# Optimization experiments

Hardware: AMD Instinct MI355X
Metric: run time of the kernel (lower is better)

The kernel has to match this reference:

```python
import jax
import jax.numpy as jnp
import numpy as np

N_NODES = 50000
N_EDGES = 1600000
D_IN = 128      # in_node_features_shape
D_EDGE = 64     # out_edge_features_shape
D_NODE = 128    # out_node_features_shape


def setup_inputs() -> dict:
    key = jax.random.key(0)
    ks = jax.random.split(key, 9)
    s = 0.05
    return {
        "node_features": jax.random.normal(ks[0], (N_NODES, D_IN), dtype=jnp.float32),
        "W_fs": jax.random.normal(ks[1], (D_IN, D_EDGE), dtype=jnp.float32) * s,
        "b_fs": jax.random.normal(ks[2], (D_EDGE,), dtype=jnp.float32) * s,
        "W_gn": jax.random.normal(ks[3], (D_IN, D_NODE), dtype=jnp.float32) * s,
        "b_gn": jax.random.normal(ks[4], (D_NODE,), dtype=jnp.float32) * s,
        "W_gin": jax.random.normal(ks[5], (D_EDGE, D_NODE), dtype=jnp.float32) * s,
        "b_gin": jax.random.normal(ks[6], (D_NODE,), dtype=jnp.float32) * s,
        "senders": jax.random.randint(ks[7], (N_EDGES,), 0, N_NODES, dtype=jnp.int32),
        "receivers": jax.random.randint(ks[8], (N_EDGES,), 0, N_NODES, dtype=jnp.int32),
    }


def reference(node_features, W_fs, b_fs, W_gn, b_gn, W_gin, b_gin, senders, receivers):
    num_nodes = node_features.shape[0]
    # f_s on all nodes, then gather by senders (matches Linear -> index_select order), then relu.
    proj = node_features @ W_fs + b_fs                      # [N, D_EDGE]
    edges = jax.nn.relu(proj[senders])                      # [E, D_EDGE]
    # scatter_max over receivers; empty segments -> 0 (torch_scatter zero-init semantics).
    agg = jax.ops.segment_max(edges, receivers, num_segments=num_nodes)  # [N, D_EDGE]
    agg = jnp.where(jnp.isfinite(agg), agg, jnp.zeros((), dtype=agg.dtype))
    nodes = (node_features @ W_gn + b_gn) + (agg @ W_gin + b_gin)        # [N, D_NODE]
    return nodes
```

## Files before the change

kernel.cpp:

```cpp
#include <hip/hip_runtime.h>

#define N_NODES 50000
#define N_EDGES 1600000
#define D_IN    128
#define D_EDGE  64
#define D_NODE  128
#define NB      32

__device__ __forceinline__ float4 fma4(float s, float4 w, float4 a) {
    a.x = fmaf(s, w.x, a.x); a.y = fmaf(s, w.y, a.y);
    a.z = fmaf(s, w.z, a.z); a.w = fmaf(s, w.w, a.w);
    return a;
}

__global__ __launch_bounds__(256)
void proj_relu_kernel(const float* __restrict__ x,
                      const float* __restrict__ W,
                      const float* __restrict__ b,
                      float* __restrict__ out) {
    __shared__ float xs[NB][D_IN + 4];
    const int tid = threadIdx.x;
    const int nb0 = blockIdx.x * NB;

    const float4* xv = (const float4*)x;
    for (int i = tid; i < NB * 32; i += 256) {
        int nl = i >> 5, c = i & 31;
        int n = nb0 + nl;
        float4 v = make_float4(0.f, 0.f, 0.f, 0.f);
        if (n < N_NODES) v = xv[(size_t)n * 32 + c];
        *(float4*)&xs[nl][c * 4] = v;
    }
    __syncthreads();

    const int fq = tid & 15;
    const int slot = tid >> 4;
    const float4* W4 = (const float4*)W;
    float4 bb = ((const float4*)b)[fq];
    float4 acc0 = bb, acc1 = bb;

#pragma unroll 8
    for (int k0 = 0; k0 < D_IN; k0 += 4) {
        float4 w0 = W4[(k0 + 0) * 16 + fq];
        float4 w1 = W4[(k0 + 1) * 16 + fq];
        float4 w2 = W4[(k0 + 2) * 16 + fq];
        float4 w3 = W4[(k0 + 3) * 16 + fq];
        float4 xa = *(const float4*)&xs[slot][k0];
        float4 xb = *(const float4*)&xs[slot + 16][k0];
        acc0 = fma4(xa.x, w0, acc0); acc0 = fma4(xa.y, w1, acc0);
        acc0 = fma4(xa.z, w2, acc0); acc0 = fma4(xa.w, w3, acc0);
        acc1 = fma4(xb.x, w0, acc1); acc1 = fma4(xb.y, w1, acc1);
        acc1 = fma4(xb.z, w2, acc1); acc1 = fma4(xb.w, w3, acc1);
    }

    float4* out4 = (float4*)out;
    int na = nb0 + slot, nbn = nb0 + slot + 16;
    if (na < N_NODES) {
        float4 r = make_float4(fmaxf(acc0.x, 0.f), fmaxf(acc0.y, 0.f),
                               fmaxf(acc0.z, 0.f), fmaxf(acc0.w, 0.f));
        out4[(size_t)na * 16 + fq] = r;
    }
    if (nbn < N_NODES) {
        float4 r = make_float4(fmaxf(acc1.x, 0.f), fmaxf(acc1.y, 0.f),
                               fmaxf(acc1.z, 0.f), fmaxf(acc1.w, 0.f));
        out4[(size_t)nbn * 16 + fq] = r;
    }
}

#define EPW 8
__global__ __launch_bounds__(256)
void scatter_max_kernel(const float* __restrict__ projR,
                        const int*   __restrict__ senders,
                        const int*   __restrict__ receivers,
                        unsigned int* __restrict__ agg_bits) {
    int tid  = blockIdx.x * blockDim.x + threadIdx.x;
    int wave = tid >> 6;
    int lane = tid & 63;
    int e0 = wave * EPW;
    if (e0 >= N_EDGES) return;

    int4 sa = *(const int4*)(senders + e0);
    int4 sb = *(const int4*)(senders + e0 + 4);
    int4 ra = *(const int4*)(receivers + e0);
    int4 rb = *(const int4*)(receivers + e0 + 4);
    int s[EPW] = {sa.x, sa.y, sa.z, sa.w, sb.x, sb.y, sb.z, sb.w};
    int r[EPW] = {ra.x, ra.y, ra.z, ra.w, rb.x, rb.y, rb.z, rb.w};

    unsigned int v[EPW];
#pragma unroll
    for (int i = 0; i < EPW; ++i)
        v[i] = __float_as_uint(projR[(size_t)s[i] * D_EDGE + lane]);

    unsigned int a[EPW];
#pragma unroll
    for (int i = 0; i < EPW; ++i)
        a[i] = agg_bits[(size_t)r[i] * D_EDGE + lane];

#pragma unroll
    for (int i = 0; i < EPW; ++i) {
        if (v[i] > a[i])
            atomicMax(agg_bits + (size_t)r[i] * D_EDGE + lane, v[i]);
    }
}

__global__ __launch_bounds__(256)
void node_out_kernel(const float* __restrict__ x,
                     const float* __restrict__ W_gn,
                     const float* __restrict__ b_gn,
                     const float* __restrict__ agg,
                     const float* __restrict__ W_gin,
                     const float* __restrict__ b_gin,
                     float* __restrict__ out) {
    __shared__ float xs[NB][D_IN + 4];
    __shared__ float as_[NB][D_EDGE + 4];
    const int tid = threadIdx.x;
    const int nb0 = blockIdx.x * NB;

    const float4* xv = (const float4*)x;
    for (int i = tid; i < NB * 32; i += 256) {
        int nl = i >> 5, c = i & 31;
        int n = nb0 + nl;
        float4 v = make_float4(0.f, 0.f, 0.f, 0.f);
        if (n < N_NODES) v = xv[(size_t)n * 32 + c];
        *(float4*)&xs[nl][c * 4] = v;
    }
    const float4* av = (const float4*)agg;
    for (int i = tid; i < NB * 16; i += 256) {
        int nl = i >> 4, c = i & 15;
        int n = nb0 + nl;
        float4 v = make_float4(0.f, 0.f, 0.f, 0.f);
        if (n < N_NODES) v = av[(size_t)n * 16 + c];
        *(float4*)&as_[nl][c * 4] = v;
    }
    __syncthreads();

    const int fq = tid & 31;
    const int slot = tid >> 5;
    const float4* Wg4 = (const float4*)W_gn;
    const float4* Wi4 = (const float4*)W_gin;
    float4 bb = ((const float4*)b_gn)[fq];
    float4 bi = ((const float4*)b_gin)[fq];
    bb.x += bi.x; bb.y += bi.y; bb.z += bi.z; bb.w += bi.w;
    float4 acc0 = bb, acc1 = bb, acc2 = bb, acc3 = bb;

#pragma unroll 4
    for (int k0 = 0; k0 < D_IN; k0 += 4) {
        float4 w0 = Wg4[(k0 + 0) * 32 + fq];
        float4 w1 = Wg4[(k0 + 1) * 32 + fq];
        float4 w2 = Wg4[(k0 + 2) * 32 + fq];
        float4 w3 = Wg4[(k0 + 3) * 32 + fq];
        float4 x0 = *(const float4*)&xs[slot][k0];
        float4 x1 = *(const float4*)&xs[slot + 8][k0];
        float4 x2 = *(const float4*)&xs[slot + 16][k0];
        float4 x3 = *(const float4*)&xs[slot + 24][k0];
        acc0 = fma4(x0.x, w0, acc0); acc0 = fma4(x0.y, w1, acc0);
        acc0 = fma4(x0.z, w2, acc0); acc0 = fma4(x0.w, w3, acc0);
        acc1 = fma4(x1.x, w0, acc1); acc1 = fma4(x1.y, w1, acc1);
        acc1 = fma4(x1.z, w2, acc1); acc1 = fma4(x1.w, w3, acc1);
        acc2 = fma4(x2.x, w0, acc2); acc2 = fma4(x2.y, w1, acc2);
        acc2 = fma4(x2.z, w2, acc2); acc2 = fma4(x2.w, w3, acc2);
        acc3 = fma4(x3.x, w0, acc3); acc3 = fma4(x3.y, w1, acc3);
        acc3 = fma4(x3.z, w2, acc3); acc3 = fma4(x3.w, w3, acc3);
    }

#pragma unroll 4
    for (int k0 = 0; k0 < D_EDGE; k0 += 4) {
        float4 w0 = Wi4[(k0 + 0) * 32 + fq];
        float4 w1 = Wi4[(k0 + 1) * 32 + fq];
        float4 w2 = Wi4[(k0 + 2) * 32 + fq];
        float4 w3 = Wi4[(k0 + 3) * 32 + fq];
        float4 x0 = *(const float4*)&as_[slot][k0];
        float4 x1 = *(const float4*)&as_[slot + 8][k0];
        float4 x2 = *(const float4*)&as_[slot + 16][k0];
        float4 x3 = *(const float4*)&as_[slot + 24][k0];
        acc0 = fma4(x0.x, w0, acc0); acc0 = fma4(x0.y, w1, acc0);
        acc0 = fma4(x0.z, w2, acc0); acc0 = fma4(x0.w, w3, acc0);
        acc1 = fma4(x1.x, w0, acc1); acc1 = fma4(x1.y, w1, acc1);
        acc1 = fma4(x1.z, w2, acc1); acc1 = fma4(x1.w, w3, acc1);
        acc2 = fma4(x2.x, w0, acc2); acc2 = fma4(x2.y, w1, acc2);
        acc2 = fma4(x2.z, w2, acc2); acc2 = fma4(x2.w, w3, acc2);
        acc3 = fma4(x3.x, w0, acc3); acc3 = fma4(x3.y, w1, acc3);
        acc3 = fma4(x3.z, w2, acc3); acc3 = fma4(x3.w, w3, acc3);
    }

    float4* out4 = (float4*)out;
    int n0 = nb0 + slot;
    if (n0 < N_NODES)          out4[(size_t)n0 * 32 + fq]        = acc0;
    if (n0 + 8 < N_NODES)      out4[(size_t)(n0 + 8) * 32 + fq]  = acc1;
    if (n0 + 16 < N_NODES)     out4[(size_t)(n0 + 16) * 32 + fq] = acc2;
    if (n0 + 24 < N_NODES)     out4[(size_t)(n0 + 24) * 32 + fq] = acc3;
}

extern "C" void kernel_launch(void* const* d_in, const int* in_sizes, int n_in,
                              void* d_out, int out_size, void* d_ws, size_t ws_size,
                              hipStream_t stream) {
    const float* node_features = (const float*)d_in[0];
    const float* W_fs          = (const float*)d_in[1];
    const float* b_fs          = (const float*)d_in[2];
    const float* W_gn          = (const float*)d_in[3];
    const float* b_gn          = (const float*)d_in[4];
    const float* W_gin         = (const float*)d_in[5];
    const float* b_gin         = (const float*)d_in[6];
    const int*   senders       = (const int*)d_in[7];
    const int*   receivers     = (const int*)d_in[8];
    float* out = (float*)d_out;

    float* projR = (float*)d_ws;
    float* agg   = projR + (size_t)N_NODES * D_EDGE;

    hipMemsetAsync(agg, 0, (size_t)N_NODES * D_EDGE * sizeof(float), stream);

    {
        int grid = (N_NODES + NB - 1) / NB;
        proj_relu_kernel<<<grid, 256, 0, stream>>>(node_features, W_fs, b_fs, projR);
    }
    {
        int waves = N_EDGES / EPW;
        int grid = (waves + 3) / 4;
        scatter_max_kernel<<<grid, 256, 0, stream>>>(projR, senders, receivers,
                                                     (unsigned int*)agg);
    }
    {
        int grid = (N_NODES + NB - 1) / NB;
        node_out_kernel<<<grid, 256, 0, stream>>>(node_features, W_gn, b_gn,
                                                  agg, W_gin, b_gin, out);
    }
}
```

Baseline: 367.4 us.

## Replace atomic scatter-max with CSR build and per-node gather-max

Replaces the per-edge atomicMax scatter into the aggregation buffer with a counting-sort CSR build: a histogram of receivers, a single-block prefix scan, and an atomic fill of sorted sender indices. One wavefront per node then gathers its incoming projected rows and reduces them with fmax in registers, writing each output row once. This removes 100M lane-level atomics and the zero memset of agg. In exchange it adds three extra kernels, 3.2M integer atomics, and a serial single-block scan, all of which run on every call.

After: 527.7 us. 1.44x slower.

```diff
diff --git a/kernel.cpp b/kernel.cpp
--- a/kernel.cpp
+++ b/kernel.cpp
@@ -66,40 +66,98 @@
     }
 }
 
-#define EPW 8
-__global__ __launch_bounds__(256)
-void scatter_max_kernel(const float* __restrict__ projR,
-                        const int*   __restrict__ senders,
-                        const int*   __restrict__ receivers,
-                        unsigned int* __restrict__ agg_bits) {
+__global__ __launch_bounds__(256)
+void hist_kernel(const int* __restrict__ receivers, int* __restrict__ counts) {
+    int i = (blockIdx.x * blockDim.x + threadIdx.x) * 4;
+    if (i >= N_EDGES) return;
+    int4 r = *(const int4*)(receivers + i);
+    atomicAdd(&counts[r.x], 1);
+    atomicAdd(&counts[r.y], 1);
+    atomicAdd(&counts[r.z], 1);
+    atomicAdd(&counts[r.w], 1);
+}
+
+__global__ __launch_bounds__(1024)
+void scan_kernel(const int* __restrict__ counts,
+                 int* __restrict__ offsets,
+                 int* __restrict__ cursor) {
+    __shared__ int sums[1024];
+    const int t = threadIdx.x;
+    const int CH = (N_NODES + 1023) / 1024;
+    int lo = t * CH;
+    int hi = lo + CH; if (hi > N_NODES) hi = N_NODES;
+    if (lo > N_NODES) lo = N_NODES;
+    int s = 0;
+    for (int i = lo; i < hi; ++i) s += counts[i];
+    sums[t] = s;
+    __syncthreads();
+    for (int d = 1; d < 1024; d <<= 1) {
+        int v = (t >= d) ? sums[t - d] : 0;
+        __syncthreads();
+        sums[t] += v;
+        __syncthreads();
+    }
+    int run = (t == 0) ? 0 : sums[t - 1];
+    for (int i = lo; i < hi; ++i) {
+        int c = counts[i];
+        offsets[i] = run;
+        cursor[i]  = run;
+        run += c;
+    }
+    if (t == 1023) offsets[N_NODES] = run;
+}
+
+__global__ __launch_bounds__(256)
+void fill_kernel(const int* __restrict__ senders,
+                 const int* __restrict__ receivers,
+                 int* __restrict__ cursor,
+                 int* __restrict__ sortedS) {
+    int i = (blockIdx.x * blockDim.x + threadIdx.x) * 4;
+    if (i >= N_EDGES) return;
+    int4 r = *(const int4*)(receivers + i);
+    int4 s = *(const int4*)(senders + i);
+    sortedS[atomicAdd(&cursor[r.x], 1)] = s.x;
+    sortedS[atomicAdd(&cursor[r.y], 1)] = s.y;
+    sortedS[atomicAdd(&cursor[r.z], 1)] = s.z;
+    sortedS[atomicAdd(&cursor[r.w], 1)] = s.w;
+}
+
+__global__ __launch_bounds__(256)
+void gather_max_kernel(const float* __restrict__ projR,
+                       const int*   __restrict__ offsets,
+                       const int*   __restrict__ sortedS,
+                       float* __restrict__ agg) {
     int tid  = blockIdx.x * blockDim.x + threadIdx.x;
-    int wave = tid >> 6;
+    int n    = tid >> 6;
     int lane = tid & 63;
-    int e0 = wave * EPW;
-    if (e0 >= N_EDGES) return;
-
-    int4 sa = *(const int4*)(senders + e0);
-    int4 sb = *(const int4*)(senders + e0 + 4);
-    int4 ra = *(const int4*)(receivers + e0);
-    int4 rb = *(const int4*)(receivers + e0 + 4);
-    int s[EPW] = {sa.x, sa.y, sa.z, sa.w, sb.x, sb.y, sb.z, sb.w};
-    int r[EPW] = {ra.x, ra.y, ra.z, ra.w, rb.x, rb.y, rb.z, rb.w};
-
-    unsigned int v[EPW];
-#pragma unroll
-    for (int i = 0; i < EPW; ++i)
-        v[i] = __float_as_uint(projR[(size_t)s[i] * D_EDGE + lane]);
-
-    unsigned int a[EPW];
-#pragma unroll
-    for (int i = 0; i < EPW; ++i)
-        a[i] = agg_bits[(size_t)r[i] * D_EDGE + lane];
-
-#pragma unroll
-    for (int i = 0; i < EPW; ++i) {
-        if (v[i] > a[i])
-            atomicMax(agg_bits + (size_t)r[i] * D_EDGE + lane, v[i]);
-    }
+    if (n >= N_NODES) return;
+    int beg = offsets[n];
+    int end = offsets[n + 1];
+    float acc = 0.0f;
+    for (int base = beg; base < end; base += 64) {
+        int len = end - base; if (len > 64) len = 64;
+        int idx = 0;
+        if (lane < len) idx = sortedS[base + lane];
+        int i = 0;
+        for (; i + 8 <= len; i += 8) {
+            float v0 = projR[(size_t)__shfl(idx, i)     * D_EDGE + lane];
+            float v1 = projR[(size_t)__shfl(idx, i + 1) * D_EDGE + lane];
+            float v2 = projR[(size_t)__shfl(idx, i + 2) * D_EDGE + lane];
+            float v3 = projR[(size_t)__shfl(idx, i + 3) * D_EDGE + lane];
+            float v4 = projR[(size_t)__shfl(idx, i + 4) * D_EDGE + lane];
+            float v5 = projR[(size_t)__shfl(idx, i + 5) * D_EDGE + lane];
+            float v6 = projR[(size_t)__shfl(idx, i + 6) * D_EDGE + lane];
+            float v7 = projR[(size_t)__shfl(idx, i + 7) * D_EDGE + lane];
+            float m0 = fmaxf(fmaxf(v0, v1), fmaxf(v2, v3));
+            float m1 = fmaxf(fmaxf(v4, v5), fmaxf(v6, v7));
+            acc = fmaxf(acc, fmaxf(m0, m1));
+        }
+        for (; i < len; ++i) {
+            int s = __shfl(idx, i);
+            acc = fmaxf(acc, projR[(size_t)s * D_EDGE + lane]);
+        }
+    }
+    agg[(size_t)n * D_EDGE + lane] = acc;
 }
 
 __global__ __launch_bounds__(256)
@@ -184,10 +242,10 @@
 
     float4* out4 = (float4*)out;
     int n0 = nb0 + slot;
-    if (n0 < N_NODES)          out4[(size_t)n0 * 32 + fq]        = acc0;
-    if (n0 + 8 < N_NODES)      out4[(size_t)(n0 + 8) * 32 + fq]  = acc1;
-    if (n0 + 16 < N_NODES)     out4[(size_t)(n0 + 16) * 32 + fq] = acc2;
-    if (n0 + 24 < N_NODES)     out4[(size_t)(n0 + 24) * 32 + fq] = acc3;
+    if (n0 < N_NODES)      out4[(size_t)n0 * 32 + fq]        = acc0;
+    if (n0 + 8 < N_NODES)  out4[(size_t)(n0 + 8) * 32 + fq]  = acc1;
+    if (n0 + 16 < N_NODES) out4[(size_t)(n0 + 16) * 32 + fq] = acc2;
+    if (n0 + 24 < N_NODES) out4[(size_t)(n0 + 24) * 32 + fq] = acc3;
 }
 
 extern "C" void kernel_launch(void* const* d_in, const int* in_sizes, int n_in,
@@ -204,20 +262,36 @@
     const int*   receivers     = (const int*)d_in[8];
     float* out = (float*)d_out;
 
-    float* projR = (float*)d_ws;
-    float* agg   = projR + (size_t)N_NODES * D_EDGE;
-
-    hipMemsetAsync(agg, 0, (size_t)N_NODES * D_EDGE * sizeof(float), stream);
+    char* p = (char*)d_ws;
+    float* projR   = (float*)p;   p += (size_t)N_NODES * D_EDGE * 4;
+    float* agg     = (float*)p;   p += (size_t)N_NODES * D_EDGE * 4;
+    int*   counts  = (int*)p;     p += (size_t)N_NODES * 4;
+    int*   offsets = (int*)p;     p += (size_t)(N_NODES + 4) * 4;
+    int*   cursor  = (int*)p;     p += (size_t)N_NODES * 4;
+    int*   sortedS = (int*)p;     p += (size_t)N_EDGES * 4;
+
+    hipMemsetAsync(counts, 0, (size_t)N_NODES * sizeof(int), stream);
 
     {
         int grid = (N_NODES + NB - 1) / NB;
         proj_relu_kernel<<<grid, 256, 0, stream>>>(node_features, W_fs, b_fs, projR);
     }
     {
-        int waves = N_EDGES / EPW;
-        int grid = (waves + 3) / 4;
-        scatter_max_kernel<<<grid, 256, 0, stream>>>(projR, senders, receivers,
-                                                     (unsigned int*)agg);
+        int threads = N_EDGES / 4;
+        hist_kernel<<<(threads + 255) / 256, 256, 0, stream>>>(receivers, counts);
+    }
+    {
+        scan_kernel<<<1, 1024, 0, stream>>>(counts, offsets, cursor);
+    }
+    {
+        int threads = N_EDGES / 4;
+        fill_kernel<<<(threads + 255) / 256, 256, 0, stream>>>(senders, receivers,
+                                                               cursor, sortedS);
+    }
+    {
+        long long threads = (long long)N_NODES * 64;
+        gather_max_kernel<<<(int)((threads + 255) / 256), 256, 0, stream>>>(
+            projR, offsets, sortedS, agg);
     }
     {
         int grid = (N_NODES + NB - 1) / NB;
```

## Replace global atomic scatter-max with receiver bucketing and shared-memory max

Applied to the files above, without the earlier changes.

Edges are counting-sorted into 1021 receiver buckets of 49 nodes each, using a per-block histogram, a scan and a fill pass that packs the local receiver and the sender into one word. Each bucket is then reduced by one block with shared-memory atomicMax, and the result is written out densely. This removes the global atomics and the memset of agg. In exchange it adds three preprocessing kernels, a single-block scan that serialises over 128 blocks, and extra traffic for the packed edge list.

After: 333.0 us. 9.4% less time.

```diff
diff --git a/kernel.cpp b/kernel.cpp
--- a/kernel.cpp
+++ b/kernel.cpp
@@ -6,6 +6,11 @@
 #define D_EDGE  64
 #define D_NODE  128
 #define NB      32
+
+#define NPB     49
+#define NBUCK   1021
+#define NBLK    128
+#define I4PB    (N_EDGES / NBLK / 4)
 
 __device__ __forceinline__ float4 fma4(float s, float4 w, float4 a) {
     a.x = fmaf(s, w.x, a.x); a.y = fmaf(s, w.y, a.y);
@@ -66,40 +71,119 @@
     }
 }
 
-#define EPW 8
-__global__ __launch_bounds__(256)
-void scatter_max_kernel(const float* __restrict__ projR,
-                        const int*   __restrict__ senders,
-                        const int*   __restrict__ receivers,
-                        unsigned int* __restrict__ agg_bits) {
-    int tid  = blockIdx.x * blockDim.x + threadIdx.x;
-    int wave = tid >> 6;
-    int lane = tid & 63;
-    int e0 = wave * EPW;
-    if (e0 >= N_EDGES) return;
-
-    int4 sa = *(const int4*)(senders + e0);
-    int4 sb = *(const int4*)(senders + e0 + 4);
-    int4 ra = *(const int4*)(receivers + e0);
-    int4 rb = *(const int4*)(receivers + e0 + 4);
-    int s[EPW] = {sa.x, sa.y, sa.z, sa.w, sb.x, sb.y, sb.z, sb.w};
-    int r[EPW] = {ra.x, ra.y, ra.z, ra.w, rb.x, rb.y, rb.z, rb.w};
-
-    unsigned int v[EPW];
-#pragma unroll
-    for (int i = 0; i < EPW; ++i)
-        v[i] = __float_as_uint(projR[(size_t)s[i] * D_EDGE + lane]);
-
-    unsigned int a[EPW];
-#pragma unroll
-    for (int i = 0; i < EPW; ++i)
-        a[i] = agg_bits[(size_t)r[i] * D_EDGE + lane];
-
-#pragma unroll
-    for (int i = 0; i < EPW; ++i) {
-        if (v[i] > a[i])
-            atomicMax(agg_bits + (size_t)r[i] * D_EDGE + lane, v[i]);
-    }
+__global__ __launch_bounds__(256)
+void bucket_hist_kernel(const int* __restrict__ receivers,
+                        int* __restrict__ hblk) {
+    __shared__ int h[NBUCK];
+    const int tid = threadIdx.x, blk = blockIdx.x;
+    for (int j = tid; j < NBUCK; j += 256) h[j] = 0;
+    __syncthreads();
+    const int4* r4 = (const int4*)receivers + (size_t)blk * I4PB;
+    for (int i = tid; i < I4PB; i += 256) {
+        int4 r = r4[i];
+        atomicAdd(&h[r.x / NPB], 1);
+        atomicAdd(&h[r.y / NPB], 1);
+        atomicAdd(&h[r.z / NPB], 1);
+        atomicAdd(&h[r.w / NPB], 1);
+    }
+    __syncthreads();
+    int* dst = hblk + (size_t)blk * NBUCK;
+    for (int j = tid; j < NBUCK; j += 256) dst[j] = h[j];
+}
+
+__global__ __launch_bounds__(1024)
+void bucket_scan_kernel(int* __restrict__ hblk, int* __restrict__ bbase) {
+    __shared__ int sums[1024];
+    const int t = threadIdx.x;
+    int cnt = 0;
+    if (t < NBUCK)
+        for (int blk = 0; blk < NBLK; ++blk) cnt += hblk[blk * NBUCK + t];
+    sums[t] = cnt;
+    __syncthreads();
+    for (int d = 1; d < 1024; d <<= 1) {
+        int v = (t >= d) ? sums[t - d] : 0;
+        __syncthreads();
+        sums[t] += v;
+        __syncthreads();
+    }
+    if (t < NBUCK) {
+        int base = sums[t] - cnt;
+        bbase[t] = base;
+        if (t == NBUCK - 1) bbase[NBUCK] = sums[t];
+        int run = base;
+        for (int blk = 0; blk < NBLK; ++blk) {
+            int idx = blk * NBUCK + t;
+            int c = hblk[idx];
+            hblk[idx] = run;
+            run += c;
+        }
+    }
+}
+
+__global__ __launch_bounds__(256)
+void bucket_fill_kernel(const int* __restrict__ senders,
+                        const int* __restrict__ receivers,
+                        const int* __restrict__ hblk,
+                        unsigned int* __restrict__ packed) {
+    __shared__ int cur[NBUCK];
+    const int tid = threadIdx.x, blk = blockIdx.x;
+    const int* src = hblk + (size_t)blk * NBUCK;
+    for (int j = tid; j < NBUCK; j += 256) cur[j] = src[j];
+    __syncthreads();
+    const int4* r4 = (const int4*)receivers + (size_t)blk * I4PB;
+    const int4* s4 = (const int4*)senders   + (size_t)blk * I4PB;
+    for (int i = tid; i < I4PB; i += 256) {
+        int4 r = r4[i];
+        int4 s = s4[i];
+        int b, rl, pos;
+        b = r.x / NPB; rl = r.x - b * NPB; pos = atomicAdd(&cur[b], 1);
+        packed[pos] = ((unsigned)rl << 17) | (unsigned)s.x;
+        b = r.y / NPB; rl = r.y - b * NPB; pos = atomicAdd(&cur[b], 1);
+        packed[pos] = ((unsigned)rl << 17) | (unsigned)s.y;
+        b = r.z / NPB; rl = r.z - b * NPB; pos = atomicAdd(&cur[b], 1);
+        packed[pos] = ((unsigned)rl << 17) | (unsigned)s.z;
+        b = r.w / NPB; rl = r.w - b * NPB; pos = atomicAdd(&cur[b], 1);
+        packed[pos] = ((unsigned)rl << 17) | (unsigned)s.w;
+    }
+}
+
+__global__ __launch_bounds__(256)
+void bucket_max_kernel(const float* __restrict__ projR,
+                       const int* __restrict__ bbase,
+                       const unsigned int* __restrict__ packed,
+                       float* __restrict__ agg) {
+    __shared__ unsigned int aggloc[NPB * D_EDGE];
+    const int tid  = threadIdx.x;
+    const int b    = blockIdx.x;
+    const int lane = tid & 63;
+    const int wid  = tid >> 6;
+    for (int i = tid; i < NPB * D_EDGE; i += 256) aggloc[i] = 0u;
+    __syncthreads();
+
+    const int beg = bbase[b], end = bbase[b + 1];
+    for (int e0 = beg + wid * 4; e0 < end; e0 += 16) {
+        int m = end - e0; if (m > 4) m = 4;
+        unsigned pk0 = packed[e0], pk1 = 0, pk2 = 0, pk3 = 0;
+        if (m > 1) pk1 = packed[e0 + 1];
+        if (m > 2) pk2 = packed[e0 + 2];
+        if (m > 3) pk3 = packed[e0 + 3];
+        float v0 = projR[(size_t)(pk0 & 0x1FFFF) * D_EDGE + lane];
+        float v1 = 0.f, v2 = 0.f, v3 = 0.f;
+        if (m > 1) v1 = projR[(size_t)(pk1 & 0x1FFFF) * D_EDGE + lane];
+        if (m > 2) v2 = projR[(size_t)(pk2 & 0x1FFFF) * D_EDGE + lane];
+        if (m > 3) v3 = projR[(size_t)(pk3 & 0x1FFFF) * D_EDGE + lane];
+        atomicMax(&aggloc[(pk0 >> 17) * D_EDGE + lane], __float_as_uint(v0));
+        if (m > 1) atomicMax(&aggloc[(pk1 >> 17) * D_EDGE + lane], __float_as_uint(v1));
+        if (m > 2) atomicMax(&aggloc[(pk2 >> 17) * D_EDGE + lane], __float_as_uint(v2));
+        if (m > 3) atomicMax(&aggloc[(pk3 >> 17) * D_EDGE + lane], __float_as_uint(v3));
+    }
+    __syncthreads();
+
+    const int n0 = b * NPB;
+    int nN = N_NODES - n0; if (nN > NPB) nN = NPB;
+    const int total = nN * D_EDGE;
+    for (int i = tid; i < total; i += 256)
+        agg[(size_t)n0 * D_EDGE + i] = __uint_as_float(aggloc[i]);
 }
 
 __global__ __launch_bounds__(256)
@@ -184,10 +268,10 @@
 
     float4* out4 = (float4*)out;
     int n0 = nb0 + slot;
-    if (n0 < N_NODES)          out4[(size_t)n0 * 32 + fq]        = acc0;
-    if (n0 + 8 < N_NODES)      out4[(size_t)(n0 + 8) * 32 + fq]  = acc1;
-    if (n0 + 16 < N_NODES)     out4[(size_t)(n0 + 16) * 32 + fq] = acc2;
-    if (n0 + 24 < N_NODES)     out4[(size_t)(n0 + 24) * 32 + fq] = acc3;
+    if (n0 < N_NODES)      out4[(size_t)n0 * 32 + fq]        = acc0;
+    if (n0 + 8 < N_NODES)  out4[(size_t)(n0 + 8) * 32 + fq]  = acc1;
+    if (n0 + 16 < N_NODES) out4[(size_t)(n0 + 16) * 32 + fq] = acc2;
+    if (n0 + 24 < N_NODES) out4[(size_t)(n0 + 24) * 32 + fq] = acc3;
 }
 
 extern "C" void kernel_launch(void* const* d_in, const int* in_sizes, int n_in,
@@ -204,21 +288,21 @@
     const int*   receivers     = (const int*)d_in[8];
     float* out = (float*)d_out;
 
-    float* projR = (float*)d_ws;
-    float* agg   = projR + (size_t)N_NODES * D_EDGE;
-
-    hipMemsetAsync(agg, 0, (size_t)N_NODES * D_EDGE * sizeof(float), stream);
+    char* p = (char*)d_ws;
+    float*        projR  = (float*)p;        p += (size_t)N_NODES * D_EDGE * 4;
+    float*        agg    = (float*)p;        p += (size_t)N_NODES * D_EDGE * 4;
+    int*          hblk   = (int*)p;          p += (size_t)NBLK * NBUCK * 4;
+    int*          bbase  = (int*)p;          p += 4096;
+    unsigned int* packed = (unsigned int*)p; p += (size_t)N_EDGES * 4;
 
     {
         int grid = (N_NODES + NB - 1) / NB;
         proj_relu_kernel<<<grid, 256, 0, stream>>>(node_features, W_fs, b_fs, projR);
     }
-    {
-        int waves = N_EDGES / EPW;
-        int grid = (waves + 3) / 4;
-        scatter_max_kernel<<<grid, 256, 0, stream>>>(projR, senders, receivers,
-                                                     (unsigned int*)agg);
-    }
+    bucket_hist_kernel<<<NBLK, 256, 0, stream>>>(receivers, hblk);
+    bucket_scan_kernel<<<1, 1024, 0, stream>>>(hblk, bbase);
+    bucket_fill_kernel<<<NBLK, 256, 0, stream>>>(senders, receivers, hblk, packed);
+    bucket_max_kernel<<<NBUCK, 256, 0, stream>>>(projR, bbase, packed, agg);
     {
         int grid = (N_NODES + NB - 1) / NB;
         node_out_kernel<<<grid, 256, 0, stream>>>(node_features, W_gn, b_gn,
```
